# Optimization experiments

Measured on AMD Instinct MI355X. Metric: run time of the kernel, lower is better.

The kernel has to match this reference:

```python
import jax, jax.numpy as jnp
import numpy as np

NUM_SPARSE = 26
VOCAB = 100000
EMB = 64
B = 2048
DENSE = 13
NUM_FEA = NUM_SPARSE + 1  # 26 embeddings + bottom-MLP output


def _xavier(key, shape):
    fan_in, fan_out = shape[0], shape[1]
    lim = jnp.sqrt(6.0 / (fan_in + fan_out))
    return jax.random.uniform(key, shape, jnp.float32, -lim, lim)


def setup_inputs() -> dict:
    key = jax.random.key(0)
    ks = jax.random.split(key, 20)
    inp = {
        "dense": jax.random.normal(ks[0], (B, DENSE), jnp.float32),
        "cat_idx": jax.random.randint(ks[1], (B, NUM_SPARSE), 0, VOCAB, jnp.int32),
        # stacked EmbeddingBag tables (all same vocab -> one [26, V, 64] tensor)
        "tables": _xavier(ks[2], (VOCAB, EMB))[None] * jnp.ones((NUM_SPARSE, 1, 1), jnp.float32) * 0
                  + jax.random.normal(ks[3], (NUM_SPARSE, VOCAB, EMB), jnp.float32) * 0.01,
        # bottom MLP: 13 -> 512 -> 256 -> 64
        "bw0": _xavier(ks[4], (DENSE, 512)), "bb0": jnp.zeros((512,), jnp.float32),
        "bw1": _xavier(ks[5], (512, 256)),   "bb1": jnp.zeros((256,), jnp.float32),
        "bw2": _xavier(ks[6], (256, EMB)),   "bb2": jnp.zeros((EMB,), jnp.float32),
        # top MLP: 415 -> 1024 -> 512 -> 256 -> 1
        "tw0": _xavier(ks[7], (EMB + NUM_FEA * (NUM_FEA - 1) // 2, 1024)), "tb0": jnp.zeros((1024,), jnp.float32),
        "tw1": _xavier(ks[8], (1024, 512)),  "tb1": jnp.zeros((512,), jnp.float32),
        "tw2": _xavier(ks[9], (512, 256)),   "tb2": jnp.zeros((256,), jnp.float32),
        "tw3": _xavier(ks[10], (256, 1)),    "tb3": jnp.zeros((1,), jnp.float32),
    }
    return inp


def reference(dense, cat_idx, tables, bw0, bb0, bw1, bb1, bw2, bb2,
              tw0, tb0, tw1, tb1, tw2, tb2, tw3, tb3):
    # bottom MLP on dense features -> [B, EMB]
    h = jax.nn.relu(dense @ bw0 + bb0)
    h = jax.nn.relu(h @ bw1 + bb1)
    bot = jax.nn.relu(h @ bw2 + bb2)

    # EmbeddingBag (single index per bag, sum mode == plain gather): [B, 26, EMB]
    feat_ids = jnp.arange(NUM_SPARSE)[None, :]  # [1, 26]
    emb = tables[feat_ids, cat_idx]             # [B, 26, EMB]

    # dot interaction: batched Gram matrix then lower-triangular gather
    T = jnp.concatenate([bot[:, None, :], emb], axis=1)  # [B, 27, EMB]
    Z = jnp.einsum("bif,bjf->bij", T, T)                  # [B, 27, 27]
    li, lj = np.tril_indices(NUM_FEA, k=-1)               # 351 pairs
    Zflat = Z[:, li, lj]                                  # [B, 351]

    R = jnp.concatenate([bot, Zflat], axis=1)             # [B, 415]

    # top MLP
    r = jax.nn.relu(R @ tw0 + tb0)
    r = jax.nn.relu(r @ tw1 + tb1)
    r = jax.nn.relu(r @ tw2 + tb2)
    out = jax.nn.sigmoid(r @ tw3 + tb3)                   # [B, 1]
    return out
```

## Files before the change

### kernel.cpp

```cpp
#include <hip/hip_runtime.h>
#include <hip/hip_bf16.h>


#define BATCH 2048
#define VOCAB 100000
#define EMB 64
#define NSPARSE 26
#define NFEA 27
#define NPAIR 351
#define RLD 448

typedef __attribute__((ext_vector_type(8))) __bf16 bf16x8;
typedef __attribute__((ext_vector_type(4))) float f32x4;
typedef __hip_bfloat16 bf16;

#define GLOAD16(g, l)                                                          \
    __builtin_amdgcn_global_load_lds(                                          \
        (const __attribute__((address_space(1))) unsigned int*)(g),            \
        (__attribute__((address_space(3))) unsigned int*)(l), 16, 0, 0)

template<int BK>
__device__ __forceinline__ int swz(int row, int s) {
    return (BK == 64) ? (s ^ (row & 7)) : (s ^ ((row >> 1) & 3));
}

template<int BK, int WR, int WC, int MREP, int NREP, bool DENSEPAD>
__global__ __launch_bounds__(256) void gemm_bf16(
    const void* __restrict__ Araw,
    const bf16* __restrict__ Wt,
    const float* __restrict__ bias,
    bf16* __restrict__ C,
    int M, int N, int K, int ldC)
{
    constexpr int BM    = WR * MREP * 16;
    constexpr int BN    = WC * NREP * 16;
    constexpr int ROWB  = BK * 2;
    constexpr int SLOTS = BK / 8;
    constexpr int KKS   = BK / 32;
    constexpr int PA    = BM * SLOTS / 256;
    constexpr int PB    = BN * SLOTS / 256;

    const int t   = threadIdx.x;
    const int nbn = N / BN;
    const int bm  = blockIdx.x / nbn;
    const int bn  = blockIdx.x % nbn;
    const int row0 = bm * BM, n0 = bn * BN;

    const int wid  = t >> 6, lane = t & 63;
    const int wr   = wid / WC, wc = wid % WC;
    const int lr   = lane & 15;
    const int q    = lane >> 4;
    const int sslot = t % SLOTS;

    f32x4 acc[MREP][NREP] = {};

    if constexpr (DENSEPAD) {
        __shared__ __align__(16) bf16 As[BM * BK];
        __shared__ __align__(16) bf16 Bs[BN * BK];

        const float* Df = (const float*)Araw;
#pragma unroll
        for (int p = 0; p < PB; ++p) {
            const int r = (p * 256 + t) / SLOTS;
            GLOAD16(Wt + (size_t)(n0 + r) * K + swz<BK>(r, sslot) * 8,
                    (char*)Bs + (p * 256 + t) * 16);
        }
#pragma unroll
        for (int idx = t; idx < BM * 32; idx += 256) {
            const int r = idx >> 5, c = idx & 31;
            const float v = (c < 13) ? Df[(size_t)(row0 + r) * 13 + c] : 0.f;
            As[r * 32 + swz<BK>(r, c >> 3) * 8 + (c & 7)] = __float2bfloat16(v);
        }
        __syncthreads();

        bf16x8 af[KKS][MREP], bfr[KKS][NREP];
#pragma unroll
        for (int kk = 0; kk < KKS; ++kk) {
#pragma unroll
            for (int m = 0; m < MREP; ++m) {
                const int r = wr * MREP * 16 + 16 * m + lr;
                af[kk][m] = *(const bf16x8*)((const char*)As + r * ROWB +
                                             swz<BK>(r, kk * 4 + q) * 16);
            }
#pragma unroll
            for (int n = 0; n < NREP; ++n) {
                const int r = wc * NREP * 16 + 16 * n + lr;
                bfr[kk][n] = *(const bf16x8*)((const char*)Bs + r * ROWB +
                                              swz<BK>(r, kk * 4 + q) * 16);
            }
        }
#pragma unroll
        for (int kk = 0; kk < KKS; ++kk)
#pragma unroll
            for (int m = 0; m < MREP; ++m)
#pragma unroll
                for (int n = 0; n < NREP; ++n)
                    acc[m][n] = __builtin_amdgcn_mfma_f32_16x16x32_bf16(
                        af[kk][m], bfr[kk][n], acc[m][n], 0, 0, 0);
    } else {
        static_assert(PA + PB == 4, "vmcnt immediate assumes 4 loads/thread");
        __shared__ __align__(16) bf16 As[3][BM * BK];
        __shared__ __align__(16) bf16 Bs[3][BN * BK];

        const bf16* Ab[PA];
        const bf16* Bb[PB];
#pragma unroll
        for (int p = 0; p < PA; ++p) {
            const int r = (p * 256 + t) / SLOTS;
            Ab[p] = (const bf16*)Araw + (size_t)(row0 + r) * K +
                    swz<BK>(r, sslot) * 8;
        }
#pragma unroll
        for (int p = 0; p < PB; ++p) {
            const int r = (p * 256 + t) / SLOTS;
            Bb[p] = Wt + (size_t)(n0 + r) * K + swz<BK>(r, sslot) * 8;
        }

        const int nsteps = K / BK;
        auto stage = [&](int s) {
            const int buf = s % 3;
            const int k0  = (s < nsteps ? s : nsteps - 1) * BK;
#pragma unroll
            for (int p = 0; p < PA; ++p)
                GLOAD16(Ab[p] + k0, (char*)As[buf] + (p * 256 + t) * 16);
#pragma unroll
            for (int p = 0; p < PB; ++p)
                GLOAD16(Bb[p] + k0, (char*)Bs[buf] + (p * 256 + t) * 16);
        };

        stage(0);
        stage(1);

        for (int ks = 0; ks < nsteps; ++ks) {
            stage(ks + 2);

            asm volatile("s_waitcnt vmcnt(8)" ::: "memory");
            __builtin_amdgcn_s_barrier();
            __builtin_amdgcn_sched_barrier(0);

            const int buf = ks % 3;
            bf16x8 af[KKS][MREP], bfr[KKS][NREP];
#pragma unroll
            for (int kk = 0; kk < KKS; ++kk) {
#pragma unroll
                for (int m = 0; m < MREP; ++m) {
                    const int r = wr * MREP * 16 + 16 * m + lr;
                    af[kk][m] = *(const bf16x8*)((const char*)As[buf] + r * ROWB +
                                                 swz<BK>(r, kk * 4 + q) * 16);
                }
#pragma unroll
                for (int n = 0; n < NREP; ++n) {
                    const int r = wc * NREP * 16 + 16 * n + lr;
                    bfr[kk][n] = *(const bf16x8*)((const char*)Bs[buf] + r * ROWB +
                                                  swz<BK>(r, kk * 4 + q) * 16);
                }
            }
#pragma unroll
            for (int kk = 0; kk < KKS; ++kk)
#pragma unroll
                for (int m = 0; m < MREP; ++m)
#pragma unroll
                    for (int n = 0; n < NREP; ++n)
                        acc[m][n] = __builtin_amdgcn_mfma_f32_16x16x32_bf16(
                            af[kk][m], bfr[kk][n], acc[m][n], 0, 0, 0);

            asm volatile("s_waitcnt lgkmcnt(0)" ::: "memory");
            __builtin_amdgcn_s_barrier();
            __builtin_amdgcn_sched_barrier(0);
        }
    }

#pragma unroll
    for (int n = 0; n < NREP; ++n) {
        const int col = n0 + wc * NREP * 16 + 16 * n + lr;
        const float bv = bias[col];
#pragma unroll
        for (int m = 0; m < MREP; ++m) {
#pragma unroll
            for (int i = 0; i < 4; ++i) {
                const int row = row0 + wr * MREP * 16 + 16 * m + q * 4 + i;
                float v = acc[m][n][i] + bv;
                v = fmaxf(v, 0.f);
                C[(size_t)row * ldC + col] = __float2bfloat16(v);
            }
        }
    }
}

struct WConvArgs {
    const float* src[6];
    bf16*        dst[6];
    int K[6], N[6], Kp[6], t0[7];
};

__global__ __launch_bounds__(256) void wconv_kernel(WConvArgs a)
{
    __shared__ float Ts[32][33];
    int w = 0;
    while (w < 5 && (int)blockIdx.x >= a.t0[w + 1]) ++w;
    const int rel = blockIdx.x - a.t0[w];
    const int K = a.K[w], N = a.N[w], Kp = a.Kp[w];
    const int nbn = N >> 5;
    const int tk = rel / nbn, tn = rel % nbn;
    const int tx = threadIdx.x & 31, ty = threadIdx.x >> 5;

    const float* src = a.src[w];
    bf16* dst = a.dst[w];

#pragma unroll
    for (int rr = 0; rr < 4; ++rr) {
        const int k = tk * 32 + ty + rr * 8;
        const int n = tn * 32 + tx;
        Ts[ty + rr * 8][tx] = (k < K) ? src[(size_t)k * N + n] : 0.f;
    }
    __syncthreads();
#pragma unroll
    for (int rr = 0; rr < 4; ++rr) {
        const int n = tn * 32 + ty + rr * 8;
        const int kp = tk * 32 + tx;
        dst[(size_t)n * Kp + kp] = __float2bfloat16(Ts[tx][ty + rr * 8]);
    }
}

__global__ __launch_bounds__(256) void interact_kernel(
    const int* __restrict__ cat_idx, const float* __restrict__ tables,
    bf16* __restrict__ R)
{
    __shared__ float T[NFEA][EMB + 1];

    const int b    = blockIdx.x;
    const int t    = threadIdx.x;
    const int g    = t >> 6;
    const int lane = t & 63;
    bf16* Rrow = R + (size_t)b * RLD;

    for (int f = g; f < NFEA; f += 4) {
        if (f == 0) {
            T[0][lane] = __bfloat162float(Rrow[lane]);
        } else {
            const int j   = f - 1;
            const int idx = cat_idx[b * NSPARSE + j];
            T[f][lane] = tables[((size_t)j * VOCAB + idx) * EMB + lane];
        }
    }
    __syncthreads();

    if (t < RLD - 415) Rrow[415 + t] = __float2bfloat16(0.f);

    for (int p = t; p < NPAIR; p += 256) {
        int i = (int)((1.0f + sqrtf(1.0f + 8.0f * (float)p)) * 0.5f);
        while (i * (i - 1) / 2 > p) --i;
        while ((i + 1) * i / 2 <= p) ++i;
        const int j = p - i * (i - 1) / 2;
        float s = 0.f;
#pragma unroll 16
        for (int k = 0; k < EMB; ++k) s += T[i][k] * T[j][k];
        Rrow[EMB + p] = __float2bfloat16(s);
    }
}

__global__ __launch_bounds__(256) void top3_kernel(
    const bf16* __restrict__ A, const float* __restrict__ w,
    const float* __restrict__ bias, float* __restrict__ out)
{
    const int gid  = blockIdx.x * 256 + threadIdx.x;
    const int row  = gid >> 6;
    const int lane = gid & 63;

    const bf16* arow = A + (size_t)row * 256;
    float s = 0.f;
#pragma unroll
    for (int k = lane; k < 256; k += 64)
        s += __bfloat162float(arow[k]) * w[k];
#pragma unroll
    for (int off = 32; off; off >>= 1) s += __shfl_down(s, off);
    if (lane == 0) out[row] = 1.f / (1.f + expf(-(s + bias[0])));
}

extern "C" void kernel_launch(void* const* d_in, const int* in_sizes, int n_in,
                              void* d_out, int out_size, void* d_ws, size_t ws_size,
                              hipStream_t stream)
{
    const float* dense   = (const float*)d_in[0];
    const int*   cat_idx = (const int*)  d_in[1];
    const float* tables  = (const float*)d_in[2];
    const float* bw0 = (const float*)d_in[3];
    const float* bb0 = (const float*)d_in[4];
    const float* bw1 = (const float*)d_in[5];
    const float* bb1 = (const float*)d_in[6];
    const float* bw2 = (const float*)d_in[7];
    const float* bb2 = (const float*)d_in[8];
    const float* tw0 = (const float*)d_in[9];
    const float* tb0 = (const float*)d_in[10];
    const float* tw1 = (const float*)d_in[11];
    const float* tb1 = (const float*)d_in[12];
    const float* tw2 = (const float*)d_in[13];
    const float* tb2 = (const float*)d_in[14];
    const float* tw3 = (const float*)d_in[15];
    const float* tb3 = (const float*)d_in[16];

    bf16* p = (bf16*)d_ws;
    bf16* h0   = p; p += (size_t)BATCH * 512;
    bf16* h1   = p; p += (size_t)BATCH * 256;
    bf16* R    = p; p += (size_t)BATCH * RLD;
    bf16* r0   = p; p += (size_t)BATCH * 1024;
    bf16* r1   = p; p += (size_t)BATCH * 512;
    bf16* r2   = p; p += (size_t)BATCH * 256;
    bf16* bw0t = p; p += 512 * 32;
    bf16* bw1t = p; p += 256 * 512;
    bf16* bw2t = p; p += 64 * 256;
    bf16* tw0t = p; p += 1024 * RLD;
    bf16* tw1t = p; p += 512 * 1024;
    bf16* tw2t = p; p += 256 * 512;
    float* out = (float*)d_out;

    WConvArgs wa;
    wa.src[0] = bw0;  wa.dst[0] = bw0t; wa.K[0] = 13;   wa.N[0] = 512;  wa.Kp[0] = 32;
    wa.src[1] = bw1;  wa.dst[1] = bw1t; wa.K[1] = 512;  wa.N[1] = 256;  wa.Kp[1] = 512;
    wa.src[2] = bw2;  wa.dst[2] = bw2t; wa.K[2] = 256;  wa.N[2] = 64;   wa.Kp[2] = 256;
    wa.src[3] = tw0;  wa.dst[3] = tw0t; wa.K[3] = 415;  wa.N[3] = 1024; wa.Kp[3] = RLD;
    wa.src[4] = tw1;  wa.dst[4] = tw1t; wa.K[4] = 1024; wa.N[4] = 512;  wa.Kp[4] = 1024;
    wa.src[5] = tw2;  wa.dst[5] = tw2t; wa.K[5] = 512;  wa.N[5] = 256;  wa.Kp[5] = 512;
    int tiles = 0;
    for (int w = 0; w < 6; ++w) {
        wa.t0[w] = tiles;
        tiles += (wa.Kp[w] >> 5) * (wa.N[w] >> 5);
    }
    wa.t0[6] = tiles;

    wconv_kernel<<<tiles, 256, 0, stream>>>(wa);

    gemm_bf16<32, 2, 2, 2, 2, true ><<<(BATCH / 64) * (512 / 64), 256, 0, stream>>>(
        dense, bw0t, bb0, h0, BATCH, 512, 32, 512);
    gemm_bf16<64, 2, 2, 2, 2, false><<<(BATCH / 64) * (256 / 64), 256, 0, stream>>>(
        h0, bw1t, bb1, h1, BATCH, 256, 512, 256);
    gemm_bf16<64, 2, 2, 2, 2, false><<<(BATCH / 64) * (64 / 64), 256, 0, stream>>>(
        h1, bw2t, bb2, R, BATCH, 64, 256, RLD);

    interact_kernel<<<BATCH, 256, 0, stream>>>(cat_idx, tables, R);

    gemm_bf16<64, 2, 2, 2, 2, false><<<(BATCH / 64) * (1024 / 64), 256, 0, stream>>>(
        R, tw0t, tb0, r0, BATCH, 1024, RLD, 1024);
    gemm_bf16<64, 2, 2, 2, 2, false><<<(BATCH / 64) * (512 / 64), 256, 0, stream>>>(
        r0, tw1t, tb1, r1, BATCH, 512, 1024, 512);
    gemm_bf16<64, 2, 2, 2, 2, false><<<(BATCH / 64) * (256 / 64), 256, 0, stream>>>(
        r1, tw2t, tb2, r2, BATCH, 256, 512, 256);
    top3_kernel<<<BATCH / 4, 256, 0, stream>>>(r2, tw3, tb3, out);
}
```

Before: 66.97 us.

## Replace pipelined GEMM with single-buffer BK=128 loop and fuse last two top layers

The GEMM template drops its triple-buffered async pipeline and uses a simple single-buffer load/sync/compute loop. The non-dense GEMMs move to BK=128 with a 16-way swizzle, and the R buffer is padded to 512 columns so K divides evenly. A new top2_kernel fuses the 512->256 layer with the final 256->1 dot product and sigmoid, removing the r2 buffer and one launch. Losing the pipeline exposes global-load latency, and the fused kernel launches only 64 blocks.

Measured after the change: 63.75 us. 4.8% less time.

```diff
diff --git a/kernel.cpp b/kernel.cpp
--- a/kernel.cpp
+++ b/kernel.cpp
@@ -4,11 +4,10 @@
 
 #define BATCH 2048
 #define VOCAB 100000
-#define EMB 64
 #define NSPARSE 26
 #define NFEA 27
 #define NPAIR 351
-#define RLD 448
+#define RLD 512
 
 typedef __attribute__((ext_vector_type(8))) __bf16 bf16x8;
 typedef __attribute__((ext_vector_type(4))) float f32x4;
@@ -21,7 +20,9 @@
 
 template<int BK>
 __device__ __forceinline__ int swz(int row, int s) {
-    return (BK == 64) ? (s ^ (row & 7)) : (s ^ ((row >> 1) & 3));
+    return (BK == 128) ? (s ^ (row & 15))
+         : (BK == 64)  ? (s ^ (row & 7))
+                       : (s ^ ((row >> 1) & 3));
 }
 
 template<int BK, int WR, int WC, int MREP, int NREP, bool DENSEPAD>
@@ -40,6 +41,9 @@
     constexpr int PA    = BM * SLOTS / 256;
     constexpr int PB    = BN * SLOTS / 256;
 
+    __shared__ __align__(16) bf16 As[BM * BK];
+    __shared__ __align__(16) bf16 Bs[BN * BK];
+
     const int t   = threadIdx.x;
     const int nbn = N / BN;
     const int bm  = blockIdx.x / nbn;
@@ -52,25 +56,41 @@
     const int q    = lane >> 4;
     const int sslot = t % SLOTS;
 
+    const bf16* Ab[PA];
+    const bf16* Bb[PB];
+#pragma unroll
+    for (int p = 0; p < PA; ++p) {
+        const int r = (p * 256 + t) / SLOTS;
+        if (!DENSEPAD)
+            Ab[p] = (const bf16*)Araw + (size_t)(row0 + r) * K +
+                    swz<BK>(r, sslot) * 8;
+    }
+#pragma unroll
+    for (int p = 0; p < PB; ++p) {
+        const int r = (p * 256 + t) / SLOTS;
+        Bb[p] = Wt + (size_t)(n0 + r) * K + swz<BK>(r, sslot) * 8;
+    }
+
     f32x4 acc[MREP][NREP] = {};
 
-    if constexpr (DENSEPAD) {
-        __shared__ __align__(16) bf16 As[BM * BK];
-        __shared__ __align__(16) bf16 Bs[BN * BK];
-
-        const float* Df = (const float*)Araw;
-#pragma unroll
-        for (int p = 0; p < PB; ++p) {
-            const int r = (p * 256 + t) / SLOTS;
-            GLOAD16(Wt + (size_t)(n0 + r) * K + swz<BK>(r, sslot) * 8,
-                    (char*)Bs + (p * 256 + t) * 16);
-        }
-#pragma unroll
-        for (int idx = t; idx < BM * 32; idx += 256) {
-            const int r = idx >> 5, c = idx & 31;
-            const float v = (c < 13) ? Df[(size_t)(row0 + r) * 13 + c] : 0.f;
-            As[r * 32 + swz<BK>(r, c >> 3) * 8 + (c & 7)] = __float2bfloat16(v);
-        }
+    for (int k0 = 0; k0 < K; k0 += BK) {
+        if constexpr (DENSEPAD) {
+            const float* Df = (const float*)Araw;
+#pragma unroll
+            for (int idx = t; idx < BM * 32; idx += 256) {
+                const int r = idx >> 5, c = idx & 31;
+                const float v = (c < 13) ? Df[(size_t)(row0 + r) * 13 + c] : 0.f;
+                As[r * 32 + swz<32>(r, c >> 3) * 8 + (c & 7)] =
+                    __float2bfloat16(v);
+            }
+        } else {
+#pragma unroll
+            for (int p = 0; p < PA; ++p)
+                GLOAD16(Ab[p] + k0, (char*)As + (p * 256 + t) * 16);
+        }
+#pragma unroll
+        for (int p = 0; p < PB; ++p)
+            GLOAD16(Bb[p] + k0, (char*)Bs + (p * 256 + t) * 16);
         __syncthreads();
 
         bf16x8 af[KKS][MREP], bfr[KKS][NREP];
@@ -97,77 +117,7 @@
                 for (int n = 0; n < NREP; ++n)
                     acc[m][n] = __builtin_amdgcn_mfma_f32_16x16x32_bf16(
                         af[kk][m], bfr[kk][n], acc[m][n], 0, 0, 0);
-    } else {
-        static_assert(PA + PB == 4, "vmcnt immediate assumes 4 loads/thread");
-        __shared__ __align__(16) bf16 As[3][BM * BK];
-        __shared__ __align__(16) bf16 Bs[3][BN * BK];
-
-        const bf16* Ab[PA];
-        const bf16* Bb[PB];
-#pragma unroll
-        for (int p = 0; p < PA; ++p) {
-            const int r = (p * 256 + t) / SLOTS;
-            Ab[p] = (const bf16*)Araw + (size_t)(row0 + r) * K +
-                    swz<BK>(r, sslot) * 8;
-        }
-#pragma unroll
-        for (int p = 0; p < PB; ++p) {
-            const int r = (p * 256 + t) / SLOTS;
-            Bb[p] = Wt + (size_t)(n0 + r) * K + swz<BK>(r, sslot) * 8;
-        }
-
-        const int nsteps = K / BK;
-        auto stage = [&](int s) {
-            const int buf = s % 3;
-            const int k0  = (s < nsteps ? s : nsteps - 1) * BK;
-#pragma unroll
-            for (int p = 0; p < PA; ++p)
-                GLOAD16(Ab[p] + k0, (char*)As[buf] + (p * 256 + t) * 16);
-#pragma unroll
-            for (int p = 0; p < PB; ++p)
-                GLOAD16(Bb[p] + k0, (char*)Bs[buf] + (p * 256 + t) * 16);
-        };
-
-        stage(0);
-        stage(1);
-
-        for (int ks = 0; ks < nsteps; ++ks) {
-            stage(ks + 2);
-
-            asm volatile("s_waitcnt vmcnt(8)" ::: "memory");
-            __builtin_amdgcn_s_barrier();
-            __builtin_amdgcn_sched_barrier(0);
-
-            const int buf = ks % 3;
-            bf16x8 af[KKS][MREP], bfr[KKS][NREP];
-#pragma unroll
-            for (int kk = 0; kk < KKS; ++kk) {
-#pragma unroll
-                for (int m = 0; m < MREP; ++m) {
-                    const int r = wr * MREP * 16 + 16 * m + lr;
-                    af[kk][m] = *(const bf16x8*)((const char*)As[buf] + r * ROWB +
-                                                 swz<BK>(r, kk * 4 + q) * 16);
-                }
-#pragma unroll
-                for (int n = 0; n < NREP; ++n) {
-                    const int r = wc * NREP * 16 + 16 * n + lr;
-                    bfr[kk][n] = *(const bf16x8*)((const char*)Bs[buf] + r * ROWB +
-                                                  swz<BK>(r, kk * 4 + q) * 16);
-                }
-            }
-#pragma unroll
-            for (int kk = 0; kk < KKS; ++kk)
-#pragma unroll
-                for (int m = 0; m < MREP; ++m)
-#pragma unroll
-                    for (int n = 0; n < NREP; ++n)
-                        acc[m][n] = __builtin_amdgcn_mfma_f32_16x16x32_bf16(
-                            af[kk][m], bfr[kk][n], acc[m][n], 0, 0, 0);
-
-            asm volatile("s_waitcnt lgkmcnt(0)" ::: "memory");
-            __builtin_amdgcn_s_barrier();
-            __builtin_amdgcn_sched_barrier(0);
-        }
+        __syncthreads();
     }
 
 #pragma unroll
@@ -179,12 +129,108 @@
 #pragma unroll
             for (int i = 0; i < 4; ++i) {
                 const int row = row0 + wr * MREP * 16 + 16 * m + q * 4 + i;
-                float v = acc[m][n][i] + bv;
-                v = fmaxf(v, 0.f);
+                float v = fmaxf(acc[m][n][i] + bv, 0.f);
                 C[(size_t)row * ldC + col] = __float2bfloat16(v);
             }
         }
     }
+}
+
+__global__ __launch_bounds__(256) void top2_kernel(
+    const bf16* __restrict__ A,
+    const bf16* __restrict__ Wt,
+    const float* __restrict__ bias,
+    const float* __restrict__ w3,
+    const float* __restrict__ b3,
+    float* __restrict__ out)
+{
+    constexpr int BK = 64, BM = 32, BN = 256, K = 512;
+    constexpr int SLOTS = 8, KKS = 2, PA = 1, PB = 8;
+
+    __shared__ __align__(16) bf16 As[BM * BK];
+    __shared__ __align__(16) bf16 Bs[BN * BK];
+    __shared__ float rsum[BM];
+
+    const int t = threadIdx.x;
+    const int row0 = blockIdx.x * BM;
+    const int wc = t >> 6, lane = t & 63;
+    const int lr = lane & 15, q = lane >> 4;
+    const int sslot = t % SLOTS;
+
+    const bf16* Ab[PA];
+    const bf16* Bb[PB];
+#pragma unroll
+    for (int p = 0; p < PA; ++p) {
+        const int r = (p * 256 + t) / SLOTS;
+        Ab[p] = A + (size_t)(row0 + r) * K + swz<BK>(r, sslot) * 8;
+    }
+#pragma unroll
+    for (int p = 0; p < PB; ++p) {
+        const int r = (p * 256 + t) / SLOTS;
+        Bb[p] = Wt + (size_t)r * K + swz<BK>(r, sslot) * 8;
+    }
+
+    f32x4 acc[2][4] = {};
+
+    for (int k0 = 0; k0 < K; k0 += BK) {
+#pragma unroll
+        for (int p = 0; p < PA; ++p)
+            GLOAD16(Ab[p] + k0, (char*)As + (p * 256 + t) * 16);
+#pragma unroll
+        for (int p = 0; p < PB; ++p)
+            GLOAD16(Bb[p] + k0, (char*)Bs + (p * 256 + t) * 16);
+        __syncthreads();
+
+        bf16x8 af[KKS][2], bfr[KKS][4];
+#pragma unroll
+        for (int kk = 0; kk < KKS; ++kk) {
+#pragma unroll
+            for (int m = 0; m < 2; ++m) {
+                const int r = 16 * m + lr;
+                af[kk][m] = *(const bf16x8*)((const char*)As + r * 128 +
+                                             swz<BK>(r, kk * 4 + q) * 16);
+            }
+#pragma unroll
+            for (int n = 0; n < 4; ++n) {
+                const int r = wc * 64 + 16 * n + lr;
+                bfr[kk][n] = *(const bf16x8*)((const char*)Bs + r * 128 +
+                                              swz<BK>(r, kk * 4 + q) * 16);
+            }
+        }
+#pragma unroll
+        for (int kk = 0; kk < KKS; ++kk)
+#pragma unroll
+            for (int m = 0; m < 2; ++m)
+#pragma unroll
+                for (int n = 0; n < 4; ++n)
+                    acc[m][n] = __builtin_amdgcn_mfma_f32_16x16x32_bf16(
+                        af[kk][m], bfr[kk][n], acc[m][n], 0, 0, 0);
+        __syncthreads();
+    }
+
+    if (t < BM) rsum[t] = 0.f;
+    __syncthreads();
+
+#pragma unroll
+    for (int m = 0; m < 2; ++m) {
+#pragma unroll
+        for (int i = 0; i < 4; ++i) {
+            float val = 0.f;
+#pragma unroll
+            for (int n = 0; n < 4; ++n) {
+                const int col = wc * 64 + 16 * n + lr;
+                val += fmaxf(acc[m][n][i] + bias[col], 0.f) * w3[col];
+            }
+            val += __shfl_xor(val, 1);
+            val += __shfl_xor(val, 2);
+            val += __shfl_xor(val, 4);
+            val += __shfl_xor(val, 8);
+            if (lr == 0) atomicAdd(&rsum[16 * m + q * 4 + i], val);
+        }
+    }
+    __syncthreads();
+    if (t < BM)
+        out[row0 + t] = 1.f / (1.f + expf(-(rsum[t] + b3[0])));
 }
 
 struct WConvArgs {
@@ -226,7 +272,7 @@
     const int* __restrict__ cat_idx, const float* __restrict__ tables,
     bf16* __restrict__ R)
 {
-    __shared__ float T[NFEA][EMB + 1];
+    __shared__ float T[NFEA][64 + 1];
 
     const int b    = blockIdx.x;
     const int t    = threadIdx.x;
@@ -240,7 +286,7 @@
         } else {
             const int j   = f - 1;
             const int idx = cat_idx[b * NSPARSE + j];
-            T[f][lane] = tables[((size_t)j * VOCAB + idx) * EMB + lane];
+            T[f][lane] = tables[((size_t)j * VOCAB + idx) * 64 + lane];
         }
     }
     __syncthreads();
@@ -254,27 +300,9 @@
         const int j = p - i * (i - 1) / 2;
         float s = 0.f;
 #pragma unroll 16
-        for (int k = 0; k < EMB; ++k) s += T[i][k] * T[j][k];
-        Rrow[EMB + p] = __float2bfloat16(s);
-    }
-}
-
-__global__ __launch_bounds__(256) void top3_kernel(
-    const bf16* __restrict__ A, const float* __restrict__ w,
-    const float* __restrict__ bias, float* __restrict__ out)
-{
-    const int gid  = blockIdx.x * 256 + threadIdx.x;
-    const int row  = gid >> 6;
-    const int lane = gid & 63;
-
-    const bf16* arow = A + (size_t)row * 256;
-    float s = 0.f;
-#pragma unroll
-    for (int k = lane; k < 256; k += 64)
-        s += __bfloat162float(arow[k]) * w[k];
-#pragma unroll
-    for (int off = 32; off; off >>= 1) s += __shfl_down(s, off);
-    if (lane == 0) out[row] = 1.f / (1.f + expf(-(s + bias[0])));
+        for (int k = 0; k < 64; ++k) s += T[i][k] * T[j][k];
+        Rrow[64 + p] = __float2bfloat16(s);
+    }
 }
 
 extern "C" void kernel_launch(void* const* d_in, const int* in_sizes, int n_in,
@@ -305,7 +333,6 @@
     bf16* R    = p; p += (size_t)BATCH * RLD;
     bf16* r0   = p; p += (size_t)BATCH * 1024;
     bf16* r1   = p; p += (size_t)BATCH * 512;
-    bf16* r2   = p; p += (size_t)BATCH * 256;
     bf16* bw0t = p; p += 512 * 32;
     bf16* bw1t = p; p += 256 * 512;
     bf16* bw2t = p; p += 64 * 256;
@@ -332,18 +359,16 @@
 
     gemm_bf16<32, 2, 2, 2, 2, true ><<<(BATCH / 64) * (512 / 64), 256, 0, stream>>>(
         dense, bw0t, bb0, h0, BATCH, 512, 32, 512);
-    gemm_bf16<64, 2, 2, 2, 2, false><<<(BATCH / 64) * (256 / 64), 256, 0, stream>>>(
+    gemm_bf16<128, 2, 2, 2, 2, false><<<(BATCH / 64) * (256 / 64), 256, 0, stream>>>(
         h0, bw1t, bb1, h1, BATCH, 256, 512, 256);
-    gemm_bf16<64, 2, 2, 2, 2, false><<<(BATCH / 64) * (64 / 64), 256, 0, stream>>>(
+    gemm_bf16<128, 2, 2, 2, 2, false><<<(BATCH / 64) * (64 / 64), 256, 0, stream>>>(
         h1, bw2t, bb2, R, BATCH, 64, 256, RLD);
 
     interact_kernel<<<BATCH, 256, 0, stream>>>(cat_idx, tables, R);
 
-    gemm_bf16<64, 2, 2, 2, 2, false><<<(BATCH / 64) * (1024 / 64), 256, 0, stream>>>(
+    gemm_bf16<128, 2, 2, 2, 2, false><<<(BATCH / 64) * (1024 / 64), 256, 0, stream>>>(
         R, tw0t, tb0, r0, BATCH, 1024, RLD, 1024);
-    gemm_bf16<64, 2, 2, 2, 2, false><<<(BATCH / 64) * (512 / 64), 256, 0, stream>>>(
+    gemm_bf16<128, 2, 2, 2, 2, false><<<(BATCH / 64) * (512 / 64), 256, 0, stream>>>(
         r0, tw1t, tb1, r1, BATCH, 512, 1024, 512);
-    gemm_bf16<64, 2, 2, 2, 2, false><<<(BATCH / 64) * (256 / 64), 256, 0, stream>>>(
-        r1, tw2t, tb2, r2, BATCH, 256, 512, 256);
-    top3_kernel<<<BATCH / 4, 256, 0, stream>>>(r2, tw3, tb3, out);
-}
+    top2_kernel<<<BATCH / 32, 256, 0, stream>>>(r1, tw2t, tb2, tw3, tb3, out);
+}
```
